# Optimization experiments

Hardware: AMD Instinct MI355X
Metric: run time of the kernel (lower is better)

The kernel has to match this reference:

```python
import jax, jax.numpy as jnp
import numpy as np
from jax import lax

B, L, N_INP, N_HID = 128, 128, 1, 2048
DT = 0.042
RHO = 0.99
INPUT_SCALING = 1.0
GAMMA_MIN, GAMMA_MAX = 2.0, 3.0
EPS_MIN, EPS_MAX = 4.0, 5.0
THETA = 0.1
ALPHA, BETA, TAU_REF = 0.3, 0.4, 0.25  # bio_cell constants


def setup_inputs() -> dict:
    rng = np.random.default_rng(0)
    x = jnp.asarray(rng.standard_normal((B, L, N_INP)), dtype=jnp.float32)
    # per-neuron gamma / epsilon drawn uniformly from (min, max) as in __init__
    gamma = jnp.asarray(rng.uniform(GAMMA_MIN, GAMMA_MAX, N_HID), dtype=jnp.float32)
    epsilon = jnp.asarray(rng.uniform(EPS_MIN, EPS_MAX, N_HID), dtype=jnp.float32)
    # h2h = 2 * (2*rand - 1), then spectral-norm scaled to radius rho
    h2h_np = 2.0 * (2.0 * rng.random((N_HID, N_HID)) - 1.0)
    eig_max = np.abs(np.linalg.eigvals(h2h_np)).max()
    h2h = jnp.asarray(h2h_np * (RHO / eig_max), dtype=jnp.float32)
    x2h = jnp.asarray(rng.random((N_INP, N_HID)) * INPUT_SCALING, dtype=jnp.float32)
    bias = jnp.asarray((rng.random(N_HID) * 2.0 - 1.0) * INPUT_SCALING, dtype=jnp.float32)
    return {"x": x, "h2h": h2h, "x2h": x2h, "bias": bias, "gamma": gamma, "epsilon": epsilon}


def reference(x, h2h, x2h, bias, gamma, epsilon):
    # bio_cell recurrence over L steps; returns mean spike rates (B, N_HID)
    dt = jnp.float32(DT)
    ref_decay = jnp.exp(jnp.float32(-DT / TAU_REF))

    def step(carry, xt):
        hy, hz, ref = carry  # each (B, N_HID); xt: (B, N_INP)
        pre = jnp.tanh(xt @ x2h + hy @ h2h + bias)
        hz = hz + dt * (pre - gamma * hy - epsilon * hz)
        hy = hy + dt * hz
        s = (hy - THETA - ref > 0).astype(hy.dtype)  # spike (non-diff)
        hy = hy * (1.0 - s * ALPHA)
        hz = hz * (1.0 - s * BETA)
        ref = ref * ref_decay + s
        return (hy, hz, ref), s

    z = jnp.zeros((x.shape[0], h2h.shape[0]), x.dtype)
    _, spikes = lax.scan(step, (z, z, z), jnp.swapaxes(x, 0, 1))  # spikes: (L, B, N_HID)
    return spikes.mean(axis=0)
```

## Files before the change

kernel.cpp:

```cpp
#include <hip/hip_runtime.h>
#include <hip/hip_bf16.h>
#include <cmath>

constexpr int   BB  = 128;
constexpr int   LL  = 128;
constexpr int   NH  = 2048;
constexpr int   KD  = 2048;
constexpr float DTc   = 0.042f;
constexpr float THETAc= 0.1f;
constexpr float ALPHAc= 0.3f;
constexpr float BETAc = 0.4f;
constexpr size_t S = (size_t)BB * NH;

typedef float f32x4 __attribute__((ext_vector_type(4)));
typedef short s16x8 __attribute__((ext_vector_type(8)));

__device__ inline ushort f2bf(float f) {
    union { __hip_bfloat16 h; ushort u; } v; v.h = __float2bfloat16(f); return v.u;
}
__device__ inline float bf2f(ushort u) {
    union { ushort u; __hip_bfloat16 h; } v; v.u = u; return __bfloat162float(v.h);
}
__device__ inline void split3(float f, ushort& b1, ushort& b2, ushort& b3) {
    b1 = f2bf(f);  float r  = f - bf2f(b1);
    b2 = f2bf(r);  float r2 = r - bf2f(b2);
    b3 = f2bf(r2);
}

__global__ __launch_bounds__(256) void packB_kernel(
    const float* __restrict__ W, ushort* __restrict__ B1,
    ushort* __restrict__ B2, ushort* __restrict__ B3)
{
    const int gw   = blockIdx.x * 4 + (threadIdx.x >> 6);
    const int lane = threadIdx.x & 63;
    const int kt = gw >> 7;
    const int nb = gw & 127;
    const size_t ob = ((size_t)(kt * 128 + nb) * 64 + lane) * 8;
    const int k0 = kt * 32 + (lane >> 4) * 8;
    const int n  = nb * 16 + (lane & 15);
    #pragma unroll
    for (int e = 0; e < 8; ++e) {
        float w = W[(size_t)(k0 + e) * NH + n];
        ushort x1, x2, x3; split3(w, x1, x2, x3);
        B1[ob + e] = x1; B2[ob + e] = x2; B3[ob + e] = x3;
    }
}

__global__ __launch_bounds__(512) void step_fused(
    const ushort* __restrict__ Ai1, const ushort* __restrict__ Ai2,
    const ushort* __restrict__ Ai3, ushort* __restrict__ Ao1,
    ushort* __restrict__ Ao2, ushort* __restrict__ Ao3,
    const ushort* __restrict__ B1, const ushort* __restrict__ B2,
    const ushort* __restrict__ B3,
    float* __restrict__ hy, float* __restrict__ hz,
    float* __restrict__ refb, float* __restrict__ ssum,
    const float* __restrict__ x, const float* __restrict__ x2h,
    const float* __restrict__ bias, const float* __restrict__ gamma,
    const float* __restrict__ eps, int t)
{
    __shared__ float Pred[8][32 * 34];
    const int tid  = threadIdx.x;
    const int lane = tid & 63;
    const int w    = tid >> 6;
    const int g    = lane >> 4;
    const int r16  = lane & 15;
    const int bid  = blockIdx.x;
    const int mb   = bid >> 6;
    const int c    = bid & 63;
    const int ktb  = w * 8;

    f32x4 acc[2][2] = {};
    const size_t aoff = (size_t)(g * 128 + mb * 32 + r16) * 8;
    const size_t boff = (size_t)(c * 128 + lane) * 8;

    #pragma unroll
    for (int j = 0; j < 8; ++j) {
        const int kt = ktb + j;
        const size_t ab = aoff + (size_t)kt * 4096;
        const size_t bb = boff + (size_t)kt * 65536;
        s16x8 a1[2], a2[2], a3[2], b1[2], b2[2], b3[2];
        #pragma unroll
        for (int mf = 0; mf < 2; ++mf) {
            a1[mf] = *(const s16x8*)(Ai1 + ab + mf * 128);
            a2[mf] = *(const s16x8*)(Ai2 + ab + mf * 128);
            a3[mf] = *(const s16x8*)(Ai3 + ab + mf * 128);
        }
        #pragma unroll
        for (int nf = 0; nf < 2; ++nf) {
            b1[nf] = *(const s16x8*)(B1 + bb + nf * 512);
            b2[nf] = *(const s16x8*)(B2 + bb + nf * 512);
            b3[nf] = *(const s16x8*)(B3 + bb + nf * 512);
        }
        #pragma unroll
        for (int mf = 0; mf < 2; ++mf)
        #pragma unroll
        for (int nf = 0; nf < 2; ++nf) {
            f32x4 cc = acc[mf][nf];
            cc = __builtin_amdgcn_mfma_f32_16x16x32_bf16(a1[mf], b1[nf], cc, 0, 0, 0);
            cc = __builtin_amdgcn_mfma_f32_16x16x32_bf16(a1[mf], b2[nf], cc, 0, 0, 0);
            cc = __builtin_amdgcn_mfma_f32_16x16x32_bf16(a2[mf], b1[nf], cc, 0, 0, 0);
            cc = __builtin_amdgcn_mfma_f32_16x16x32_bf16(a1[mf], b3[nf], cc, 0, 0, 0);
            cc = __builtin_amdgcn_mfma_f32_16x16x32_bf16(a2[mf], b2[nf], cc, 0, 0, 0);
            cc = __builtin_amdgcn_mfma_f32_16x16x32_bf16(a3[mf], b1[nf], cc, 0, 0, 0);
            acc[mf][nf] = cc;
        }
    }

    #pragma unroll
    for (int mf = 0; mf < 2; ++mf)
    #pragma unroll
    for (int nf = 0; nf < 2; ++nf)
    #pragma unroll
    for (int r = 0; r < 4; ++r)
        Pred[w][(mf * 16 + g * 4 + r) * 34 + nf * 16 + r16] = acc[mf][nf][r];

    __syncthreads();

    const int e0  = tid * 2;
    const int row = e0 >> 5;
    const int col = e0 & 31;
    const int b   = mb * 32 + row;
    const int n0  = c * 32 + col, n1 = n0 + 1;

    float pa0 = 0.f, pa1 = 0.f;
    #pragma unroll
    for (int q = 0; q < 8; ++q) {
        const float2 pv = *(const float2*)&Pred[q][row * 34 + col];
        pa0 += pv.x; pa1 += pv.y;
    }

    const size_t ig = (size_t)b * NH + n0;
    const float xt = x[(size_t)b * LL + t];
    const float rd = expf(-DTc / 0.25f);
    const float2 x2hv = *(const float2*)(x2h + n0);
    const float2 biv  = *(const float2*)(bias + n0);
    const float2 gav  = *(const float2*)(gamma + n0);
    const float2 epv  = *(const float2*)(eps + n0);
    float2 hyv = *(float2*)(hy + ig);
    float2 hzv = *(float2*)(hz + ig);
    float2 rfv = *(float2*)(refb + ig);
    float2 ssv = *(float2*)(ssum + ig);

    {
        float pre = tanhf(pa0 + xt * x2hv.x + biv.x);
        hzv.x += DTc * (pre - gav.x * hyv.x - epv.x * hzv.x);
        hyv.x += DTc * hzv.x;
        float s = (hyv.x - THETAc - rfv.x > 0.f) ? 1.f : 0.f;
        hyv.x *= 1.f - s * ALPHAc;
        hzv.x *= 1.f - s * BETAc;
        rfv.x = rfv.x * rd + s;
        ssv.x += s;
        ushort u1, u2, u3; split3(hyv.x, u1, u2, u3);
        const int kt0 = n0 >> 5, gg = (n0 >> 3) & 3, ee = n0 & 7;
        const size_t o = ((size_t)(kt0 * 4 + gg) * 128 + b) * 8 + ee;
        Ao1[o] = u1; Ao2[o] = u2; Ao3[o] = u3;
    }
    {
        float pre = tanhf(pa1 + xt * x2hv.y + biv.y);
        hzv.y += DTc * (pre - gav.y * hyv.y - epv.y * hzv.y);
        hyv.y += DTc * hzv.y;
        float s = (hyv.y - THETAc - rfv.y > 0.f) ? 1.f : 0.f;
        hyv.y *= 1.f - s * ALPHAc;
        hzv.y *= 1.f - s * BETAc;
        rfv.y = rfv.y * rd + s;
        ssv.y += s;
        ushort u1, u2, u3; split3(hyv.y, u1, u2, u3);
        const int kt1 = n1 >> 5, gg = (n1 >> 3) & 3, ee = n1 & 7;
        const size_t o = ((size_t)(kt1 * 4 + gg) * 128 + b) * 8 + ee;
        Ao1[o] = u1; Ao2[o] = u2; Ao3[o] = u3;
    }

    *(float2*)(hy + ig)   = hyv;
    *(float2*)(hz + ig)   = hzv;
    *(float2*)(refb + ig) = rfv;
    *(float2*)(ssum + ig) = ssv;
}

__global__ __launch_bounds__(512) void finish_kernel(const float* __restrict__ ssum,
                                                     float* __restrict__ out)
{
    const int i = blockIdx.x * 512 + threadIdx.x;
    out[i] = ssum[i] * (1.0f / (float)LL);
}

template<int KCH>
__global__ __launch_bounds__(512) void gemm_vec(
    const float* __restrict__ hy_in, float* __restrict__ P,
    const float* __restrict__ W)
{
    const int lane = threadIdx.x & 63;
    const int w    = __builtin_amdgcn_readfirstlane((int)(threadIdx.x >> 6));
    const int n        = blockIdx.x * 64 + lane;
    const int rowbase  = blockIdx.y * 64 + w * 8;
    const int kq       = blockIdx.z;
    const int k0       = kq * KCH;
    const float* __restrict__ hp = hy_in + (size_t)rowbase * KD + k0;
    const float* __restrict__ Wp = W + (size_t)k0 * NH + n;
    float acc[8] = {0.f,0.f,0.f,0.f,0.f,0.f,0.f,0.f};
    float wc[8], w1[8], w2[8];
    #pragma unroll
    for (int i = 0; i < 8; ++i) w1[i] = Wp[(size_t)i * NH];
    {
        const float* Wq = Wp + (size_t)8 * NH;
        #pragma unroll
        for (int i = 0; i < 8; ++i) w2[i] = Wq[(size_t)i * NH];
    }
    for (int k = 0; k < KCH; k += 8) {
        #pragma unroll
        for (int i = 0; i < 8; ++i) wc[i] = w1[i];
        #pragma unroll
        for (int i = 0; i < 8; ++i) w1[i] = w2[i];
        if (k + 16 < KCH) {
            const float* Wq = Wp + (size_t)(k + 16) * NH;
            #pragma unroll
            for (int i = 0; i < 8; ++i) w2[i] = Wq[(size_t)i * NH];
        }
        #pragma unroll
        for (int j = 0; j < 8; ++j) {
            const float* hr = hp + (size_t)j * KD + k;
            float4 a = *(const float4*)(hr);
            float4 bq = *(const float4*)(hr + 4);
            acc[j] = fmaf(a.x, wc[0], acc[j]);  acc[j] = fmaf(a.y, wc[1], acc[j]);
            acc[j] = fmaf(a.z, wc[2], acc[j]);  acc[j] = fmaf(a.w, wc[3], acc[j]);
            acc[j] = fmaf(bq.x, wc[4], acc[j]); acc[j] = fmaf(bq.y, wc[5], acc[j]);
            acc[j] = fmaf(bq.z, wc[6], acc[j]); acc[j] = fmaf(bq.w, wc[7], acc[j]);
        }
    }
    float* Pp = P + ((size_t)kq * BB + rowbase) * NH + n;
    #pragma unroll
    for (int j = 0; j < 8; ++j) Pp[(size_t)j * NH] = acc[j];
}

__global__ __launch_bounds__(256) void update_vec(
    const float* __restrict__ P, int kqn, const float* __restrict__ hy_in,
    float* __restrict__ hy_out, float* __restrict__ hz,
    float* __restrict__ refb, float* __restrict__ ssum,
    const float* __restrict__ x2h, const float* __restrict__ bias,
    const float* __restrict__ gamma, const float* __restrict__ eps,
    const float* __restrict__ x, int t)
{
    const int i = blockIdx.x * 256 + threadIdx.x;
    const int b = i >> 11;
    const int n = i & (NH - 1);
    float acc = 0.f;
    for (int q = 0; q < kqn; ++q) acc += P[(size_t)q * S + i];
    const float xt = x[(size_t)b * LL + t];
    float pre = tanhf(acc + xt * x2h[n] + bias[n]);
    float hyv = hy_in[i];
    float hzv = hz[i];
    float rf  = refb[i];
    const float rd = expf(-DTc / 0.25f);
    hzv += DTc * (pre - gamma[n] * hyv - eps[n] * hzv);
    hyv += DTc * hzv;
    float s = (hyv - THETAc - rf > 0.f) ? 1.f : 0.f;
    hyv *= 1.f - s * ALPHAc;
    hzv *= 1.f - s * BETAc;
    rf = rf * rd + s;
    hy_out[i] = hyv; hz[i] = hzv; refb[i] = rf; ssum[i] += s;
}

extern "C" void kernel_launch(void* const* d_in, const int* in_sizes, int n_in,
                              void* d_out, int out_size, void* d_ws, size_t ws_size,
                              hipStream_t stream) {
    const float* x     = (const float*)d_in[0];
    const float* W     = (const float*)d_in[1];
    const float* x2h   = (const float*)d_in[2];
    const float* bias  = (const float*)d_in[3];
    const float* gamma = (const float*)d_in[4];
    const float* eps   = (const float*)d_in[5];
    float* out = (float*)d_out;

    const size_t SB = S * sizeof(float);

    const size_t offSt  = 3 * S * 2;
    const size_t offAb  = offSt + 4 * SB;
    const size_t offB   = offAb + 3 * S * 2;
    const size_t need   = offB + 3 * (16 * S) * 2;

    if (ws_size >= need) {
        char* base = (char*)d_ws;
        ushort* Aa1 = (ushort*)base;
        ushort* Aa2 = Aa1 + S;
        ushort* Aa3 = Aa2 + S;
        float*  hy = (float*)(base + offSt);
        float*  hz = hy + S;
        float*  rf = hz + S;
        float*  ss = rf + S;
        ushort* Ab1 = (ushort*)(base + offAb);
        ushort* Ab2 = Ab1 + S;
        ushort* Ab3 = Ab2 + S;
        ushort* B1 = (ushort*)(base + offB);
        ushort* B2 = B1 + 16 * S;
        ushort* B3 = B2 + 16 * S;

        hipMemsetAsync(d_ws, 0, offAb, stream);

        packB_kernel<<<2048, 256, 0, stream>>>(W, B1, B2, B3);

        ushort *i1 = Aa1, *i2 = Aa2, *i3 = Aa3, *o1 = Ab1, *o2 = Ab2, *o3 = Ab3;
        for (int t = 0; t < LL; ++t) {
            step_fused<<<256, 512, 0, stream>>>(i1, i2, i3, o1, o2, o3,
                                                B1, B2, B3, hy, hz, rf, ss,
                                                x, x2h, bias, gamma, eps, t);
            ushort* tp;
            tp = i1; i1 = o1; o1 = tp;
            tp = i2; i2 = o2; o2 = tp;
            tp = i3; i3 = o3; o3 = tp;
        }
        finish_kernel<<<(unsigned)(S / 512), 512, 0, stream>>>(ss, out);
    } else {
        float* ws = (float*)d_ws;
        float* hyA = ws;
        float* hz  = ws + S;
        float* rf  = ws + 2 * S;
        float* ss  = ws + 3 * S;
        float* hyB = ws + 4 * S;
        float* P   = ws + 5 * S;
        const int kq = (ws_size >= 13 * SB) ? 8 : 4;
        hipMemsetAsync(d_ws, 0, 4 * SB, stream);
        dim3 ggrid(NH / 64, BB / 64, kq);
        const float* hin = hyA;
        float* hout = hyB;
        for (int t = 0; t < LL; ++t) {
            if (kq == 8)
                gemm_vec<KD / 8><<<ggrid, 512, 0, stream>>>(hin, P, W);
            else
                gemm_vec<KD / 4><<<ggrid, 512, 0, stream>>>(hin, P, W);
            update_vec<<<(unsigned)(S / 256), 256, 0, stream>>>(
                P, kq, hin, hout, hz, rf, ss, x2h, bias, gamma, eps, x, t);
            const float* tmp = hout; hout = (float*)hin; hin = tmp;
        }
        finish_kernel<<<(unsigned)(S / 512), 512, 0, stream>>>(ss, out);
    }
}
```

Measured before the change: 1.799 ms.

## Interleave bf16 split planes and double-buffer fragment loads in fused step

Packs the three bf16 split components of the weights and the hidden state into one interleaved array (24 shorts per lane) instead of three separate planes, so each fragment's hi/mid/lo parts sit contiguously. The MFMA loop now prefetches the next k-tile's fragments into a second register set while the current one is consumed, and the state/parameter loads are hoisted ahead of the GEMM so their latency overlaps it. The aim is better memory locality and load/compute overlap, at the cost of roughly doubling the registers held for fragments, which may reduce occupancy.

```diff
diff --git a/kernel.cpp b/kernel.cpp
--- a/kernel.cpp
+++ b/kernel.cpp
@@ -28,30 +28,26 @@
 }
 
 __global__ __launch_bounds__(256) void packB_kernel(
-    const float* __restrict__ W, ushort* __restrict__ B1,
-    ushort* __restrict__ B2, ushort* __restrict__ B3)
+    const float* __restrict__ W, ushort* __restrict__ Bp)
 {
     const int gw   = blockIdx.x * 4 + (threadIdx.x >> 6);
     const int lane = threadIdx.x & 63;
     const int kt = gw >> 7;
     const int nb = gw & 127;
-    const size_t ob = ((size_t)(kt * 128 + nb) * 64 + lane) * 8;
+    const size_t ob = ((size_t)(kt * 128 + nb) * 64 + lane) * 24;
     const int k0 = kt * 32 + (lane >> 4) * 8;
     const int n  = nb * 16 + (lane & 15);
     #pragma unroll
     for (int e = 0; e < 8; ++e) {
         float w = W[(size_t)(k0 + e) * NH + n];
         ushort x1, x2, x3; split3(w, x1, x2, x3);
-        B1[ob + e] = x1; B2[ob + e] = x2; B3[ob + e] = x3;
+        Bp[ob + e] = x1; Bp[ob + 8 + e] = x2; Bp[ob + 16 + e] = x3;
     }
 }
 
 __global__ __launch_bounds__(512) void step_fused(
-    const ushort* __restrict__ Ai1, const ushort* __restrict__ Ai2,
-    const ushort* __restrict__ Ai3, ushort* __restrict__ Ao1,
-    ushort* __restrict__ Ao2, ushort* __restrict__ Ao3,
-    const ushort* __restrict__ B1, const ushort* __restrict__ B2,
-    const ushort* __restrict__ B3,
+    const ushort* __restrict__ Ai, ushort* __restrict__ Ao,
+    const ushort* __restrict__ Bp,
     float* __restrict__ hy, float* __restrict__ hz,
     float* __restrict__ refb, float* __restrict__ ssum,
     const float* __restrict__ x, const float* __restrict__ x2h,
@@ -69,69 +65,13 @@
     const int c    = bid & 63;
     const int ktb  = w * 8;
 
-    f32x4 acc[2][2] = {};
-    const size_t aoff = (size_t)(g * 128 + mb * 32 + r16) * 8;
-    const size_t boff = (size_t)(c * 128 + lane) * 8;
-
-    #pragma unroll
-    for (int j = 0; j < 8; ++j) {
-        const int kt = ktb + j;
-        const size_t ab = aoff + (size_t)kt * 4096;
-        const size_t bb = boff + (size_t)kt * 65536;
-        s16x8 a1[2], a2[2], a3[2], b1[2], b2[2], b3[2];
-        #pragma unroll
-        for (int mf = 0; mf < 2; ++mf) {
-            a1[mf] = *(const s16x8*)(Ai1 + ab + mf * 128);
-            a2[mf] = *(const s16x8*)(Ai2 + ab + mf * 128);
-            a3[mf] = *(const s16x8*)(Ai3 + ab + mf * 128);
-        }
-        #pragma unroll
-        for (int nf = 0; nf < 2; ++nf) {
-            b1[nf] = *(const s16x8*)(B1 + bb + nf * 512);
-            b2[nf] = *(const s16x8*)(B2 + bb + nf * 512);
-            b3[nf] = *(const s16x8*)(B3 + bb + nf * 512);
-        }
-        #pragma unroll
-        for (int mf = 0; mf < 2; ++mf)
-        #pragma unroll
-        for (int nf = 0; nf < 2; ++nf) {
-            f32x4 cc = acc[mf][nf];
-            cc = __builtin_amdgcn_mfma_f32_16x16x32_bf16(a1[mf], b1[nf], cc, 0, 0, 0);
-            cc = __builtin_amdgcn_mfma_f32_16x16x32_bf16(a1[mf], b2[nf], cc, 0, 0, 0);
-            cc = __builtin_amdgcn_mfma_f32_16x16x32_bf16(a2[mf], b1[nf], cc, 0, 0, 0);
-            cc = __builtin_amdgcn_mfma_f32_16x16x32_bf16(a1[mf], b3[nf], cc, 0, 0, 0);
-            cc = __builtin_amdgcn_mfma_f32_16x16x32_bf16(a2[mf], b2[nf], cc, 0, 0, 0);
-            cc = __builtin_amdgcn_mfma_f32_16x16x32_bf16(a3[mf], b1[nf], cc, 0, 0, 0);
-            acc[mf][nf] = cc;
-        }
-    }
-
-    #pragma unroll
-    for (int mf = 0; mf < 2; ++mf)
-    #pragma unroll
-    for (int nf = 0; nf < 2; ++nf)
-    #pragma unroll
-    for (int r = 0; r < 4; ++r)
-        Pred[w][(mf * 16 + g * 4 + r) * 34 + nf * 16 + r16] = acc[mf][nf][r];
-
-    __syncthreads();
-
     const int e0  = tid * 2;
     const int row = e0 >> 5;
     const int col = e0 & 31;
     const int b   = mb * 32 + row;
     const int n0  = c * 32 + col, n1 = n0 + 1;
-
-    float pa0 = 0.f, pa1 = 0.f;
-    #pragma unroll
-    for (int q = 0; q < 8; ++q) {
-        const float2 pv = *(const float2*)&Pred[q][row * 34 + col];
-        pa0 += pv.x; pa1 += pv.y;
-    }
-
     const size_t ig = (size_t)b * NH + n0;
     const float xt = x[(size_t)b * LL + t];
-    const float rd = expf(-DTc / 0.25f);
     const float2 x2hv = *(const float2*)(x2h + n0);
     const float2 biv  = *(const float2*)(bias + n0);
     const float2 gav  = *(const float2*)(gamma + n0);
@@ -141,6 +81,78 @@
     float2 rfv = *(float2*)(refb + ig);
     float2 ssv = *(float2*)(ssum + ig);
 
+    f32x4 acc[2][2] = {};
+    const size_t abase = ((size_t)((ktb * 4 + g) * 128) + mb * 32 + r16) * 24;
+    const size_t bbase = ((size_t)(ktb * 128 + c * 2) * 64 + lane) * 24;
+
+    s16x8 aC[2][3], bC[2][3], aN[2][3], bN[2][3];
+
+    #define LDF(j, AA, BB) do { \
+        const size_t ab_ = abase + (size_t)(j) * 12288; \
+        const size_t bb_ = bbase + (size_t)(j) * 196608; \
+        _Pragma("unroll") \
+        for (int mf = 0; mf < 2; ++mf) { \
+            _Pragma("unroll") \
+            for (int s = 0; s < 3; ++s) \
+                AA[mf][s] = *(const s16x8*)(Ai + ab_ + mf * 384 + s * 8); \
+        } \
+        _Pragma("unroll") \
+        for (int nf = 0; nf < 2; ++nf) { \
+            _Pragma("unroll") \
+            for (int s = 0; s < 3; ++s) \
+                BB[nf][s] = *(const s16x8*)(Bp + bb_ + nf * 1536 + s * 8); \
+        } \
+    } while (0)
+
+    LDF(0, aC, bC);
+    #pragma unroll
+    for (int j = 0; j < 8; ++j) {
+        if (j < 7) {
+            if (j & 1) LDF(j + 1, aC, bC); else LDF(j + 1, aN, bN);
+        }
+        #pragma unroll
+        for (int mf = 0; mf < 2; ++mf)
+        #pragma unroll
+        for (int nf = 0; nf < 2; ++nf) {
+            f32x4 cc = acc[mf][nf];
+            if (j & 1) {
+                cc = __builtin_amdgcn_mfma_f32_16x16x32_bf16(aN[mf][0], bN[nf][0], cc, 0, 0, 0);
+                cc = __builtin_amdgcn_mfma_f32_16x16x32_bf16(aN[mf][0], bN[nf][1], cc, 0, 0, 0);
+                cc = __builtin_amdgcn_mfma_f32_16x16x32_bf16(aN[mf][1], bN[nf][0], cc, 0, 0, 0);
+                cc = __builtin_amdgcn_mfma_f32_16x16x32_bf16(aN[mf][0], bN[nf][2], cc, 0, 0, 0);
+                cc = __builtin_amdgcn_mfma_f32_16x16x32_bf16(aN[mf][1], bN[nf][1], cc, 0, 0, 0);
+                cc = __builtin_amdgcn_mfma_f32_16x16x32_bf16(aN[mf][2], bN[nf][0], cc, 0, 0, 0);
+            } else {
+                cc = __builtin_amdgcn_mfma_f32_16x16x32_bf16(aC[mf][0], bC[nf][0], cc, 0, 0, 0);
+                cc = __builtin_amdgcn_mfma_f32_16x16x32_bf16(aC[mf][0], bC[nf][1], cc, 0, 0, 0);
+                cc = __builtin_amdgcn_mfma_f32_16x16x32_bf16(aC[mf][1], bC[nf][0], cc, 0, 0, 0);
+                cc = __builtin_amdgcn_mfma_f32_16x16x32_bf16(aC[mf][0], bC[nf][2], cc, 0, 0, 0);
+                cc = __builtin_amdgcn_mfma_f32_16x16x32_bf16(aC[mf][1], bC[nf][1], cc, 0, 0, 0);
+                cc = __builtin_amdgcn_mfma_f32_16x16x32_bf16(aC[mf][2], bC[nf][0], cc, 0, 0, 0);
+            }
+            acc[mf][nf] = cc;
+        }
+    }
+    #undef LDF
+
+    #pragma unroll
+    for (int mf = 0; mf < 2; ++mf)
+    #pragma unroll
+    for (int nf = 0; nf < 2; ++nf)
+    #pragma unroll
+    for (int r = 0; r < 4; ++r)
+        Pred[w][(mf * 16 + g * 4 + r) * 34 + nf * 16 + r16] = acc[mf][nf][r];
+
+    __syncthreads();
+
+    float pa0 = 0.f, pa1 = 0.f;
+    #pragma unroll
+    for (int q = 0; q < 8; ++q) {
+        const float2 pv = *(const float2*)&Pred[q][row * 34 + col];
+        pa0 += pv.x; pa1 += pv.y;
+    }
+
+    const float rd = expf(-DTc / 0.25f);
     {
         float pre = tanhf(pa0 + xt * x2hv.x + biv.x);
         hzv.x += DTc * (pre - gav.x * hyv.x - epv.x * hzv.x);
@@ -152,8 +164,8 @@
         ssv.x += s;
         ushort u1, u2, u3; split3(hyv.x, u1, u2, u3);
         const int kt0 = n0 >> 5, gg = (n0 >> 3) & 3, ee = n0 & 7;
-        const size_t o = ((size_t)(kt0 * 4 + gg) * 128 + b) * 8 + ee;
-        Ao1[o] = u1; Ao2[o] = u2; Ao3[o] = u3;
+        const size_t o = ((size_t)(kt0 * 4 + gg) * 128 + b) * 24 + ee;
+        Ao[o] = u1; Ao[o + 8] = u2; Ao[o + 16] = u3;
     }
     {
         float pre = tanhf(pa1 + xt * x2hv.y + biv.y);
@@ -166,8 +178,8 @@
         ssv.y += s;
         ushort u1, u2, u3; split3(hyv.y, u1, u2, u3);
         const int kt1 = n1 >> 5, gg = (n1 >> 3) & 3, ee = n1 & 7;
-        const size_t o = ((size_t)(kt1 * 4 + gg) * 128 + b) * 8 + ee;
-        Ao1[o] = u1; Ao2[o] = u2; Ao3[o] = u3;
+        const size_t o = ((size_t)(kt1 * 4 + gg) * 128 + b) * 24 + ee;
+        Ao[o] = u1; Ao[o + 8] = u2; Ao[o + 16] = u3;
     }
 
     *(float2*)(hy + ig)   = hyv;
@@ -275,37 +287,27 @@
     const size_t offSt  = 3 * S * 2;
     const size_t offAb  = offSt + 4 * SB;
     const size_t offB   = offAb + 3 * S * 2;
-    const size_t need   = offB + 3 * (16 * S) * 2;
+    const size_t need   = offB + 48 * S * 2;
 
     if (ws_size >= need) {
         char* base = (char*)d_ws;
-        ushort* Aa1 = (ushort*)base;
-        ushort* Aa2 = Aa1 + S;
-        ushort* Aa3 = Aa2 + S;
+        ushort* Aa = (ushort*)base;
         float*  hy = (float*)(base + offSt);
         float*  hz = hy + S;
         float*  rf = hz + S;
         float*  ss = rf + S;
-        ushort* Ab1 = (ushort*)(base + offAb);
-        ushort* Ab2 = Ab1 + S;
-        ushort* Ab3 = Ab2 + S;
-        ushort* B1 = (ushort*)(base + offB);
-        ushort* B2 = B1 + 16 * S;
-        ushort* B3 = B2 + 16 * S;
+        ushort* Ab = (ushort*)(base + offAb);
+        ushort* Bp = (ushort*)(base + offB);
 
         hipMemsetAsync(d_ws, 0, offAb, stream);
 
-        packB_kernel<<<2048, 256, 0, stream>>>(W, B1, B2, B3);
-
-        ushort *i1 = Aa1, *i2 = Aa2, *i3 = Aa3, *o1 = Ab1, *o2 = Ab2, *o3 = Ab3;
+        packB_kernel<<<2048, 256, 0, stream>>>(W, Bp);
+
+        ushort *ai = Aa, *ao = Ab;
         for (int t = 0; t < LL; ++t) {
-            step_fused<<<256, 512, 0, stream>>>(i1, i2, i3, o1, o2, o3,
-                                                B1, B2, B3, hy, hz, rf, ss,
+            step_fused<<<256, 512, 0, stream>>>(ai, ao, Bp, hy, hz, rf, ss,
                                                 x, x2h, bias, gamma, eps, t);
-            ushort* tp;
-            tp = i1; i1 = o1; o1 = tp;
-            tp = i2; i2 = o2; o2 = tp;
-            tp = i3; i3 = o3; o3 = tp;
+            ushort* tp = ai; ai = ao; ao = tp;
         }
         finish_kernel<<<(unsigned)(S / 512), 512, 0, stream>>>(ss, out);
     } else {
```

After: 2.244 ms. 24.7% more time.
